# Optimization experiments

Measured on AMD Instinct MI355X. Metric: run time of the kernel, lower is better.

## Reference

```python
import jax, jax.numpy as jnp
import numpy as np

BATCH, N_IN, N_OUT, D = 32768, 256, 256, 8

def setup_inputs() -> dict:
    key = jax.random.key(0)
    k1, k2 = jax.random.split(key)
    noise_std = 1.0 / (N_IN * (D + 1))
    x = jax.random.normal(k1, (BATCH, N_IN), dtype=jnp.float32)
    c_basis = noise_std * jax.random.normal(k2, (N_OUT, N_IN, D + 1), dtype=jnp.float32)
    c_act = jnp.ones((N_OUT, N_IN), dtype=jnp.float32)
    return {"x": x, "c_basis": c_basis, "c_act": c_act}

def _cheby_basis(x, degree):
    # x: (batch, n_in) -> (batch, n_in, degree+1) Chebyshev T_k(tanh(x))
    t = jnp.tanh(x)
    polys = [jnp.ones_like(t), t]
    for _ in range(2, degree + 1):
        polys.append(2.0 * t * polys[-1] - polys[-2])
    return jnp.stack(polys[: degree + 1], axis=-1)

def reference(x, c_basis, c_act):
    batch = x.shape[0]
    n_out = c_basis.shape[0]
    degree = c_basis.shape[-1] - 1
    Ti = _cheby_basis(x, degree)                      # (batch, n_in, D+1)
    cheb = Ti.reshape(batch, -1)                      # (batch, n_in*(D+1))
    cheb_w = (c_basis * c_act[..., None]).reshape(n_out, -1)
    return jnp.matmul(cheb, cheb_w.T)                 # (batch, n_out)
```

## Files before the change

kernel.cpp:

```cpp
#include <hip/hip_runtime.h>
#include <hip/hip_bf16.h>

#define BATCH 32768
#define NIN   256
#define NOUT  256

typedef __attribute__((ext_vector_type(8))) short bf16x8;
typedef __attribute__((ext_vector_type(4))) float f32x4;
typedef __attribute__((ext_vector_type(2))) float f32x2;
typedef __attribute__((ext_vector_type(4))) unsigned int u32x4;

static __device__ __forceinline__ unsigned short bf16_rne(float f) {
  unsigned u = __float_as_uint(f);
  u += 0x7fffu + ((u >> 16) & 1u);
  return (unsigned short)(u >> 16);
}

static __device__ __forceinline__ float fast_tanh(float v) {
  float a = fabsf(v);
  float z = __expf(-2.0f * a);
  float r = (1.0f - z) * __builtin_amdgcn_rcpf(1.0f + z);
  return copysignf(r, v);
}

static __device__ __forceinline__ unsigned pack_pair(f32x2 v) {
  __hip_bfloat162 h2 = __float22bfloat162_rn(make_float2(v[0], v[1]));
  union { __hip_bfloat162 h; unsigned u; } cv;
  cv.h = h2;
  return cv.u;
}

static __device__ __forceinline__ void init_state(const f32x4 x0, const f32x4 x1,
                                                  f32x2* cur, f32x2* prev,
                                                  f32x2* t2) {
  #pragma unroll
  for (int p = 0; p < 4; ++p) {
    float va = (p < 2) ? x0[2 * p]     : x1[2 * p - 4];
    float vb = (p < 2) ? x0[2 * p + 1] : x1[2 * p - 3];
    float ta = fast_tanh(va);
    float tb = fast_tanh(vb);
    cur[p]  = (f32x2){ta, tb};
    t2[p]   = cur[p] + cur[p];
    prev[p] = (f32x2){1.0f, 1.0f};
  }
}

static __device__ __forceinline__ void phase_barrier() {
  __builtin_amdgcn_sched_barrier(0);
  __builtin_amdgcn_s_barrier();
  __builtin_amdgcn_sched_barrier(0);
}

__global__ void cheby_prepack(const float* __restrict__ cb,
                              const float* __restrict__ ca,
                              unsigned short* __restrict__ Bp) {
  int tid = blockIdx.x * 256 + threadIdx.x;
  int j    = tid & 7;
  int col  = (tid >> 3) & 15;
  int kg   = (tid >> 7) & 3;
  int tile = (tid >> 9) & 15;
  int ic   = (tid >> 13) & 7;
  int dm   = tid >> 16;
  int i = ic * 32 + kg * 8 + j;
  int n = tile * 16 + col;
  float w = cb[n * (NIN * 9) + i * 9 + (dm + 1)] * ca[n * NIN + i];
  Bp[tid] = bf16_rne(w);
}

__global__ void cheby_bias(const float* __restrict__ cb,
                           const float* __restrict__ ca,
                           float* __restrict__ bias) {
  int n = blockIdx.x;
  int l = threadIdx.x;
  float s = 0.0f;
  #pragma unroll
  for (int k = 0; k < 4; ++k) {
    int i = l + k * 64;
    s += cb[n * (NIN * 9) + i * 9] * ca[n * NIN + i];
  }
  #pragma unroll
  for (int off = 32; off; off >>= 1) s += __shfl_down(s, off);
  if (l == 0) bias[n] = s;
}

__global__ __launch_bounds__(512, 2)
void cheby_mfma(const float* __restrict__ x,
                const unsigned short* __restrict__ Bp,
                const float* __restrict__ bias,
                float* __restrict__ out) {
  __shared__ unsigned short Asm[2][8][8][512];

  int tid  = threadIdx.x;
  int w    = tid >> 6;
  int lane = tid & 63;
  int row16 = lane & 15;
  int kg    = lane >> 4;

  int wr = w >> 2;
  int wc = w & 3;
  int base_row = blockIdx.x * 128;
  int tile0    = wc * 4;

  const float* xw = x + (size_t)(base_row + w * 16 + row16) * NIN + kg * 8;
  char* wbase = (char*)Asm + (w * 1024 + lane * 16);
  const char* abase   = (const char*)Asm + lane * 16;
  const char* bp_lane = (const char*)Bp + kg * 256 + row16 * 16;

  f32x4 acc[4][4];
  #pragma unroll
  for (int a = 0; a < 4; ++a)
    #pragma unroll
    for (int b = 0; b < 4; ++b) acc[a][b] = (f32x4)0.0f;

  f32x4 xa = *(const f32x4*)xw;
  f32x4 xb = *(const f32x4*)(xw + 4);
  {
    f32x2 c0[4], p0[4], t0[4];
    init_state(xa, xb, c0, p0, t0);
    #pragma unroll
    for (int d = 1; d <= 8; ++d) {
      u32x4 pk;
      #pragma unroll
      for (int q = 0; q < 4; ++q) pk[q] = pack_pair(c0[q]);
      *(u32x4*)(wbase + (d - 1) * 8192) = pk;
      if (d < 8) {
        #pragma unroll
        for (int q = 0; q < 4; ++q) {
          f32x2 nx = __builtin_elementwise_fma(t0[q], c0[q], -p0[q]);
          p0[q] = c0[q];
          c0[q] = nx;
        }
      }
    }
  }
  xa = *(const f32x4*)(xw + 32);
  xb = *(const f32x4*)(xw + 36);
  f32x2 cur[4], prev[4], t2[4];
  init_state(xa, xb, cur, prev, t2);

  bf16x8 af[2][4], bfr[2][4];
  {
    const char* bp0 = bp_lane + (size_t)tile0 * 1024;
    #pragma unroll
    for (int nt = 0; nt < 4; ++nt)
      bfr[0][nt] = *(const bf16x8*)(bp0 + nt * 1024);
  }
  __builtin_amdgcn_sched_barrier(0);
  asm volatile("s_waitcnt lgkmcnt(0)" ::: "memory");
  __builtin_amdgcn_s_barrier();
  __builtin_amdgcn_sched_barrier(0);
  #pragma unroll
  for (int mt = 0; mt < 4; ++mt)
    af[0][mt] = *(const bf16x8*)(abase + (wr * 4 + mt) * 1024);

  for (int ic = 0; ic < 7; ++ic) {
    const char* ai   = abase + (ic & 1) * 65536 + (wr * 4) * 1024;
    const char* ain  = abase + ((ic + 1) & 1) * 65536 + (wr * 4) * 1024;
    char*       wp   = wbase + ((ic + 1) & 1) * 65536;
    const char* bpi  = bp_lane + (size_t)(ic * 16 + tile0) * 1024;
    const char* bpin = bp_lane + (size_t)((ic + 1) * 16 + tile0) * 1024;

    #pragma unroll
    for (int p = 0; p < 8; ++p) {
      if (p < 7) {
        #pragma unroll
        for (int mt = 0; mt < 4; ++mt)
          af[(p + 1) & 1][mt] =
              *(const bf16x8*)(ai + (p + 1) * 8192 + mt * 1024);
      } else {
        #pragma unroll
        for (int mt = 0; mt < 4; ++mt)
          af[0][mt] = *(const bf16x8*)(ain + mt * 1024);
      }
      if (p < 7) {
        #pragma unroll
        for (int nt = 0; nt < 4; ++nt)
          bfr[(p + 1) & 1][nt] =
              *(const bf16x8*)(bpi + (size_t)(p + 1) * 131072 + nt * 1024);
      } else {
        #pragma unroll
        for (int nt = 0; nt < 4; ++nt)
          bfr[0][nt] = *(const bf16x8*)(bpin + nt * 1024);
      }
      {
        u32x4 pk;
        #pragma unroll
        for (int q = 0; q < 4; ++q) pk[q] = pack_pair(cur[q]);
        *(u32x4*)(wp + p * 8192) = pk;
        if (p < 7) {
          #pragma unroll
          for (int q = 0; q < 4; ++q) {
            f32x2 nx = __builtin_elementwise_fma(t2[q], cur[q], -prev[q]);
            prev[q] = cur[q];
            cur[q]  = nx;
          }
        }
      }
      if (p == 3 && ic <= 5) {
        xa = *(const f32x4*)(xw + (ic + 2) * 32);
        xb = *(const f32x4*)(xw + (ic + 2) * 32 + 4);
      }
      if (p == 7 && ic <= 5)
        init_state(xa, xb, cur, prev, t2);

      phase_barrier();

      __builtin_amdgcn_s_setprio(1);
      #pragma unroll
      for (int mt = 0; mt < 4; ++mt)
        #pragma unroll
        for (int nt = 0; nt < 4; ++nt)
          acc[mt][nt] = __builtin_amdgcn_mfma_f32_16x16x32_bf16(
              af[p & 1][mt], bfr[p & 1][nt], acc[mt][nt], 0, 0, 0);
      __builtin_amdgcn_s_setprio(0);
    }
  }

  {
    const char* ai  = abase + 65536 + (wr * 4) * 1024;
    const char* bpi = bp_lane + (size_t)(7 * 16 + tile0) * 1024;
    #pragma unroll
    for (int p = 0; p < 8; ++p) {
      if (p < 7) {
        #pragma unroll
        for (int mt = 0; mt < 4; ++mt)
          af[(p + 1) & 1][mt] =
              *(const bf16x8*)(ai + (p + 1) * 8192 + mt * 1024);
        #pragma unroll
        for (int nt = 0; nt < 4; ++nt)
          bfr[(p + 1) & 1][nt] =
              *(const bf16x8*)(bpi + (size_t)(p + 1) * 131072 + nt * 1024);
      }
      __builtin_amdgcn_s_setprio(1);
      #pragma unroll
      for (int mt = 0; mt < 4; ++mt)
        #pragma unroll
        for (int nt = 0; nt < 4; ++nt)
          acc[mt][nt] = __builtin_amdgcn_mfma_f32_16x16x32_bf16(
              af[p & 1][mt], bfr[p & 1][nt], acc[mt][nt], 0, 0, 0);
      __builtin_amdgcn_s_setprio(0);
    }
  }

  #pragma unroll
  for (int nt = 0; nt < 4; ++nt) {
    int c = (tile0 + nt) * 16 + row16;
    float bv = bias[c];
    #pragma unroll
    for (int mt = 0; mt < 4; ++mt) {
      int r0 = base_row + wr * 64 + mt * 16 + kg * 4;
      #pragma unroll
      for (int q = 0; q < 4; ++q)
        out[(size_t)(r0 + q) * NOUT + c] = acc[mt][nt][q] + bv;
    }
  }
}

extern "C" void kernel_launch(void* const* d_in, const int* in_sizes, int n_in,
                              void* d_out, int out_size, void* d_ws, size_t ws_size,
                              hipStream_t stream) {
  const float* x  = (const float*)d_in[0];
  const float* cb = (const float*)d_in[1];
  const float* ca = (const float*)d_in[2];
  float* out = (float*)d_out;

  unsigned short* Bp = (unsigned short*)d_ws;
  float* bias = (float*)((char*)d_ws + 8 * NIN * NOUT * 2);

  cheby_prepack<<<(8 * NIN * NOUT) / 256, 256, 0, stream>>>(cb, ca, Bp);
  cheby_bias<<<NOUT, 64, 0, stream>>>(cb, ca, bias);
  cheby_mfma<<<256, 512, 0, stream>>>(x, Bp, bias, out);
}
```

Measured before the change: 47.75 us.

## Process two Chebyshev degrees per barrier phase, halving block barriers

The main loop now handles two degrees per phase (4 phases instead of 8 per input chunk), so each barrier is followed by 32 MFMAs instead of 16. Global B fragments are prefetched two degrees ahead in a double buffer. The A fragments are no longer software-pipelined one phase ahead: they are loaded at the start of each phase and waited on with lgkmcnt(0) right after the barrier. This cuts barrier count and increases MFMA work per sync, at the cost of more registers (B buffer doubles) and exposed LDS read latency before the MFMAs.

Result: slower. 49.43 us (+3.5%).

```diff
diff --git a/kernel.cpp b/kernel.cpp
--- a/kernel.cpp
+++ b/kernel.cpp
@@ -43,12 +43,6 @@
     t2[p]   = cur[p] + cur[p];
     prev[p] = (f32x2){1.0f, 1.0f};
   }
-}
-
-static __device__ __forceinline__ void phase_barrier() {
-  __builtin_amdgcn_sched_barrier(0);
-  __builtin_amdgcn_s_barrier();
-  __builtin_amdgcn_sched_barrier(0);
 }
 
 __global__ void cheby_prepack(const float* __restrict__ cb,
@@ -138,56 +132,59 @@
   f32x2 cur[4], prev[4], t2[4];
   init_state(xa, xb, cur, prev, t2);
 
-  bf16x8 af[2][4], bfr[2][4];
+  bf16x8 bfr[2][2][4];
   {
     const char* bp0 = bp_lane + (size_t)tile0 * 1024;
     #pragma unroll
-    for (int nt = 0; nt < 4; ++nt)
-      bfr[0][nt] = *(const bf16x8*)(bp0 + nt * 1024);
+    for (int dd = 0; dd < 2; ++dd)
+      #pragma unroll
+      for (int nt = 0; nt < 4; ++nt)
+        bfr[0][dd][nt] =
+            *(const bf16x8*)(bp0 + (size_t)dd * 131072 + nt * 1024);
   }
   __builtin_amdgcn_sched_barrier(0);
   asm volatile("s_waitcnt lgkmcnt(0)" ::: "memory");
   __builtin_amdgcn_s_barrier();
   __builtin_amdgcn_sched_barrier(0);
-  #pragma unroll
-  for (int mt = 0; mt < 4; ++mt)
-    af[0][mt] = *(const bf16x8*)(abase + (wr * 4 + mt) * 1024);
 
   for (int ic = 0; ic < 7; ++ic) {
     const char* ai   = abase + (ic & 1) * 65536 + (wr * 4) * 1024;
-    const char* ain  = abase + ((ic + 1) & 1) * 65536 + (wr * 4) * 1024;
     char*       wp   = wbase + ((ic + 1) & 1) * 65536;
     const char* bpi  = bp_lane + (size_t)(ic * 16 + tile0) * 1024;
     const char* bpin = bp_lane + (size_t)((ic + 1) * 16 + tile0) * 1024;
 
     #pragma unroll
-    for (int p = 0; p < 8; ++p) {
-      if (p < 7) {
-        #pragma unroll
-        for (int mt = 0; mt < 4; ++mt)
-          af[(p + 1) & 1][mt] =
-              *(const bf16x8*)(ai + (p + 1) * 8192 + mt * 1024);
+    for (int ph = 0; ph < 4; ++ph) {
+      const int d0 = ph * 2;
+      bf16x8 af[2][4];
+      #pragma unroll
+      for (int dd = 0; dd < 2; ++dd)
+        #pragma unroll
+        for (int mt = 0; mt < 4; ++mt)
+          af[dd][mt] =
+              *(const bf16x8*)(ai + (d0 + dd) * 8192 + mt * 1024);
+      if (ph < 3) {
+        #pragma unroll
+        for (int dd = 0; dd < 2; ++dd)
+          #pragma unroll
+          for (int nt = 0; nt < 4; ++nt)
+            bfr[(ph + 1) & 1][dd][nt] = *(const bf16x8*)(
+                bpi + (size_t)(d0 + 2 + dd) * 131072 + nt * 1024);
       } else {
         #pragma unroll
-        for (int mt = 0; mt < 4; ++mt)
-          af[0][mt] = *(const bf16x8*)(ain + mt * 1024);
-      }
-      if (p < 7) {
-        #pragma unroll
-        for (int nt = 0; nt < 4; ++nt)
-          bfr[(p + 1) & 1][nt] =
-              *(const bf16x8*)(bpi + (size_t)(p + 1) * 131072 + nt * 1024);
-      } else {
-        #pragma unroll
-        for (int nt = 0; nt < 4; ++nt)
-          bfr[0][nt] = *(const bf16x8*)(bpin + nt * 1024);
-      }
-      {
+        for (int dd = 0; dd < 2; ++dd)
+          #pragma unroll
+          for (int nt = 0; nt < 4; ++nt)
+            bfr[0][dd][nt] = *(const bf16x8*)(
+                bpin + (size_t)dd * 131072 + nt * 1024);
+      }
+      #pragma unroll
+      for (int s = 0; s < 2; ++s) {
         u32x4 pk;
         #pragma unroll
         for (int q = 0; q < 4; ++q) pk[q] = pack_pair(cur[q]);
-        *(u32x4*)(wp + p * 8192) = pk;
-        if (p < 7) {
+        *(u32x4*)(wp + (d0 + s) * 8192) = pk;
+        if (d0 + s < 7) {
           #pragma unroll
           for (int q = 0; q < 4; ++q) {
             f32x2 nx = __builtin_elementwise_fma(t2[q], cur[q], -prev[q]);
@@ -196,22 +193,27 @@
           }
         }
       }
-      if (p == 3 && ic <= 5) {
+      if (ph == 1 && ic <= 5) {
         xa = *(const f32x4*)(xw + (ic + 2) * 32);
         xb = *(const f32x4*)(xw + (ic + 2) * 32 + 4);
       }
-      if (p == 7 && ic <= 5)
+      if (ph == 3 && ic <= 5)
         init_state(xa, xb, cur, prev, t2);
 
-      phase_barrier();
+      __builtin_amdgcn_sched_barrier(0);
+      __builtin_amdgcn_s_barrier();
+      asm volatile("s_waitcnt lgkmcnt(0)" ::: "memory");
+      __builtin_amdgcn_sched_barrier(0);
 
       __builtin_amdgcn_s_setprio(1);
       #pragma unroll
-      for (int mt = 0; mt < 4; ++mt)
-        #pragma unroll
-        for (int nt = 0; nt < 4; ++nt)
-          acc[mt][nt] = __builtin_amdgcn_mfma_f32_16x16x32_bf16(
-              af[p & 1][mt], bfr[p & 1][nt], acc[mt][nt], 0, 0, 0);
+      for (int dd = 0; dd < 2; ++dd)
+        #pragma unroll
+        for (int mt = 0; mt < 4; ++mt)
+          #pragma unroll
+          for (int nt = 0; nt < 4; ++nt)
+            acc[mt][nt] = __builtin_amdgcn_mfma_f32_16x16x32_bf16(
+                af[dd][mt], bfr[ph & 1][dd][nt], acc[mt][nt], 0, 0, 0);
       __builtin_amdgcn_s_setprio(0);
     }
   }
@@ -220,24 +222,32 @@
     const char* ai  = abase + 65536 + (wr * 4) * 1024;
     const char* bpi = bp_lane + (size_t)(7 * 16 + tile0) * 1024;
     #pragma unroll
-    for (int p = 0; p < 8; ++p) {
-      if (p < 7) {
-        #pragma unroll
-        for (int mt = 0; mt < 4; ++mt)
-          af[(p + 1) & 1][mt] =
-              *(const bf16x8*)(ai + (p + 1) * 8192 + mt * 1024);
-        #pragma unroll
-        for (int nt = 0; nt < 4; ++nt)
-          bfr[(p + 1) & 1][nt] =
-              *(const bf16x8*)(bpi + (size_t)(p + 1) * 131072 + nt * 1024);
+    for (int ph = 0; ph < 4; ++ph) {
+      const int d0 = ph * 2;
+      bf16x8 af[2][4];
+      #pragma unroll
+      for (int dd = 0; dd < 2; ++dd)
+        #pragma unroll
+        for (int mt = 0; mt < 4; ++mt)
+          af[dd][mt] =
+              *(const bf16x8*)(ai + (d0 + dd) * 8192 + mt * 1024);
+      if (ph < 3) {
+        #pragma unroll
+        for (int dd = 0; dd < 2; ++dd)
+          #pragma unroll
+          for (int nt = 0; nt < 4; ++nt)
+            bfr[(ph + 1) & 1][dd][nt] = *(const bf16x8*)(
+                bpi + (size_t)(d0 + 2 + dd) * 131072 + nt * 1024);
       }
       __builtin_amdgcn_s_setprio(1);
       #pragma unroll
-      for (int mt = 0; mt < 4; ++mt)
-        #pragma unroll
-        for (int nt = 0; nt < 4; ++nt)
-          acc[mt][nt] = __builtin_amdgcn_mfma_f32_16x16x32_bf16(
-              af[p & 1][mt], bfr[p & 1][nt], acc[mt][nt], 0, 0, 0);
+      for (int dd = 0; dd < 2; ++dd)
+        #pragma unroll
+        for (int mt = 0; mt < 4; ++mt)
+          #pragma unroll
+          for (int nt = 0; nt < 4; ++nt)
+            acc[mt][nt] = __builtin_amdgcn_mfma_f32_16x16x32_bf16(
+                af[dd][mt], bfr[ph & 1][dd][nt], acc[mt][nt], 0, 0, 0);
       __builtin_amdgcn_s_setprio(0);
     }
   }
```

## Switch MFMA tiles from 16x16x32 to 32x32x16 with matching A/B layouts

Applied to the files above, without the earlier changes.

Replaces the 4x4 grid of 16x16x32 bf16 MFMAs per wave with a 2x2 grid of 32x32x16 MFMAs over two K chunks. The prepacked weight layout, the LDS A-tile layout and the epilogue row mapping change to match the 32-row fragment shape. The larger instruction is meant to issue fewer MFMAs per phase and give each fragment load more reuse. In exchange it adds new index math and a different accumulator register layout.

New measurement: 51.37 us. 1.08x slower.

```diff
diff --git a/kernel.cpp b/kernel.cpp
--- a/kernel.cpp
+++ b/kernel.cpp
@@ -5,10 +5,11 @@
 #define NIN   256
 #define NOUT  256
 
-typedef __attribute__((ext_vector_type(8))) short bf16x8;
-typedef __attribute__((ext_vector_type(4))) float f32x4;
-typedef __attribute__((ext_vector_type(2))) float f32x2;
-typedef __attribute__((ext_vector_type(4))) unsigned int u32x4;
+typedef __attribute__((ext_vector_type(8)))  short bf16x8;
+typedef __attribute__((ext_vector_type(4)))  float f32x4;
+typedef __attribute__((ext_vector_type(16))) float f32x16;
+typedef __attribute__((ext_vector_type(2)))  float f32x2;
+typedef __attribute__((ext_vector_type(4)))  unsigned int u32x4;
 
 static __device__ __forceinline__ unsigned short bf16_rne(float f) {
   unsigned u = __float_as_uint(f);
@@ -55,14 +56,16 @@
                               const float* __restrict__ ca,
                               unsigned short* __restrict__ Bp) {
   int tid = blockIdx.x * 256 + threadIdx.x;
-  int j    = tid & 7;
-  int col  = (tid >> 3) & 15;
-  int kg   = (tid >> 7) & 3;
-  int tile = (tid >> 9) & 15;
-  int ic   = (tid >> 13) & 7;
-  int dm   = tid >> 16;
-  int i = ic * 32 + kg * 8 + j;
-  int n = tile * 16 + col;
+  int j      = tid & 7;
+  int fl     = (tid >> 3) & 63;
+  int chunk  = (tid >> 9) & 1;
+  int tile32 = (tid >> 10) & 7;
+  int ic     = (tid >> 13) & 7;
+  int dm     = (tid >> 16) & 7;
+  int col = fl & 31;
+  int kh  = fl >> 5;
+  int n = tile32 * 32 + col;
+  int i = ic * 32 + chunk * 16 + kh * 8 + j;
   float w = cb[n * (NIN * 9) + i * 9 + (dm + 1)] * ca[n * NIN + i];
   Bp[tid] = bf16_rne(w);
 }
@@ -88,29 +91,27 @@
                 const unsigned short* __restrict__ Bp,
                 const float* __restrict__ bias,
                 float* __restrict__ out) {
-  __shared__ unsigned short Asm[2][8][8][512];
+  __shared__ unsigned short Asm_[2][8][4][2][512];
 
   int tid  = threadIdx.x;
   int w    = tid >> 6;
   int lane = tid & 63;
-  int row16 = lane & 15;
-  int kg    = lane >> 4;
 
   int wr = w >> 2;
   int wc = w & 3;
   int base_row = blockIdx.x * 128;
-  int tile0    = wc * 4;
-
-  const float* xw = x + (size_t)(base_row + w * 16 + row16) * NIN + kg * 8;
-  char* wbase = (char*)Asm + (w * 1024 + lane * 16);
-  const char* abase   = (const char*)Asm + lane * 16;
-  const char* bp_lane = (const char*)Bp + kg * 256 + row16 * 16;
-
-  f32x4 acc[4][4];
-  #pragma unroll
-  for (int a = 0; a < 4; ++a)
-    #pragma unroll
-    for (int b = 0; b < 4; ++b) acc[a][b] = (f32x4)0.0f;
+
+  const float* xw = x + (size_t)(base_row + ((tid >> 7) << 5) + (tid & 31)) * NIN
+                      + ((tid >> 5) & 3) * 8;
+  char* wbase = (char*)Asm_ + tid * 16;
+  const char* abase   = (const char*)Asm_ + lane * 16;
+  const char* bp_lane = (const char*)Bp + lane * 16;
+
+  f32x16 acc[2][2];
+  #pragma unroll
+  for (int a = 0; a < 2; ++a)
+    #pragma unroll
+    for (int b = 0; b < 2; ++b) acc[a][b] = (f32x16)0.0f;
 
   f32x4 xa = *(const f32x4*)xw;
   f32x4 xb = *(const f32x4*)(xw + 4);
@@ -118,12 +119,12 @@
     f32x2 c0[4], p0[4], t0[4];
     init_state(xa, xb, c0, p0, t0);
     #pragma unroll
-    for (int d = 1; d <= 8; ++d) {
+    for (int d = 0; d < 8; ++d) {
       u32x4 pk;
       #pragma unroll
       for (int q = 0; q < 4; ++q) pk[q] = pack_pair(c0[q]);
-      *(u32x4*)(wbase + (d - 1) * 8192) = pk;
-      if (d < 8) {
+      *(u32x4*)(wbase + d * 8192) = pk;
+      if (d < 7) {
         #pragma unroll
         for (int q = 0; q < 4; ++q) {
           f32x2 nx = __builtin_elementwise_fma(t0[q], c0[q], -p0[q]);
@@ -138,49 +139,64 @@
   f32x2 cur[4], prev[4], t2[4];
   init_state(xa, xb, cur, prev, t2);
 
-  bf16x8 af[2][4], bfr[2][4];
+  bf16x8 af[2][2][2], bfr[2][2][2];
   {
-    const char* bp0 = bp_lane + (size_t)tile0 * 1024;
-    #pragma unroll
-    for (int nt = 0; nt < 4; ++nt)
-      bfr[0][nt] = *(const bf16x8*)(bp0 + nt * 1024);
+    const char* bp0 = bp_lane + (size_t)(wc * 4) * 1024;
+    #pragma unroll
+    for (int ch = 0; ch < 2; ++ch)
+      #pragma unroll
+      for (int nt = 0; nt < 2; ++nt)
+        bfr[0][ch][nt] = *(const bf16x8*)(bp0 + (nt * 2 + ch) * 1024);
   }
   __builtin_amdgcn_sched_barrier(0);
   asm volatile("s_waitcnt lgkmcnt(0)" ::: "memory");
   __builtin_amdgcn_s_barrier();
   __builtin_amdgcn_sched_barrier(0);
   #pragma unroll
-  for (int mt = 0; mt < 4; ++mt)
-    af[0][mt] = *(const bf16x8*)(abase + (wr * 4 + mt) * 1024);
+  for (int mt = 0; mt < 2; ++mt)
+    #pragma unroll
+    for (int ch = 0; ch < 2; ++ch)
+      af[0][mt][ch] =
+          *(const bf16x8*)(abase + (wr * 2 + mt) * 2048 + ch * 1024);
 
   for (int ic = 0; ic < 7; ++ic) {
-    const char* ai   = abase + (ic & 1) * 65536 + (wr * 4) * 1024;
-    const char* ain  = abase + ((ic + 1) & 1) * 65536 + (wr * 4) * 1024;
+    const char* ai   = abase + (ic & 1) * 65536;
+    const char* ain  = abase + ((ic + 1) & 1) * 65536;
     char*       wp   = wbase + ((ic + 1) & 1) * 65536;
-    const char* bpi  = bp_lane + (size_t)(ic * 16 + tile0) * 1024;
-    const char* bpin = bp_lane + (size_t)((ic + 1) * 16 + tile0) * 1024;
+    const char* bpi  = bp_lane + (size_t)(ic * 16 + wc * 4) * 1024;
+    const char* bpin = bp_lane + (size_t)((ic + 1) * 16 + wc * 4) * 1024;
 
     #pragma unroll
     for (int p = 0; p < 8; ++p) {
       if (p < 7) {
         #pragma unroll
-        for (int mt = 0; mt < 4; ++mt)
-          af[(p + 1) & 1][mt] =
-              *(const bf16x8*)(ai + (p + 1) * 8192 + mt * 1024);
+        for (int mt = 0; mt < 2; ++mt)
+          #pragma unroll
+          for (int ch = 0; ch < 2; ++ch)
+            af[(p + 1) & 1][mt][ch] = *(const bf16x8*)(
+                ai + (p + 1) * 8192 + (wr * 2 + mt) * 2048 + ch * 1024);
       } else {
         #pragma unroll
-        for (int mt = 0; mt < 4; ++mt)
-          af[0][mt] = *(const bf16x8*)(ain + mt * 1024);
+        for (int mt = 0; mt < 2; ++mt)
+          #pragma unroll
+          for (int ch = 0; ch < 2; ++ch)
+            af[0][mt][ch] = *(const bf16x8*)(
+                ain + (wr * 2 + mt) * 2048 + ch * 1024);
       }
       if (p < 7) {
         #pragma unroll
-        for (int nt = 0; nt < 4; ++nt)
-          bfr[(p + 1) & 1][nt] =
-              *(const bf16x8*)(bpi + (size_t)(p + 1) * 131072 + nt * 1024);
+        for (int ch = 0; ch < 2; ++ch)
+          #pragma unroll
+          for (int nt = 0; nt < 2; ++nt)
+            bfr[(p + 1) & 1][ch][nt] = *(const bf16x8*)(
+                bpi + (size_t)(p + 1) * 131072 + (nt * 2 + ch) * 1024);
       } else {
         #pragma unroll
-        for (int nt = 0; nt < 4; ++nt)
-          bfr[0][nt] = *(const bf16x8*)(bpin + nt * 1024);
+        for (int ch = 0; ch < 2; ++ch)
+          #pragma unroll
+          for (int nt = 0; nt < 2; ++nt)
+            bfr[0][ch][nt] =
+                *(const bf16x8*)(bpin + (nt * 2 + ch) * 1024);
       }
       {
         u32x4 pk;
@@ -207,51 +223,61 @@
 
       __builtin_amdgcn_s_setprio(1);
       #pragma unroll
-      for (int mt = 0; mt < 4; ++mt)
-        #pragma unroll
-        for (int nt = 0; nt < 4; ++nt)
-          acc[mt][nt] = __builtin_amdgcn_mfma_f32_16x16x32_bf16(
-              af[p & 1][mt], bfr[p & 1][nt], acc[mt][nt], 0, 0, 0);
+      for (int ch = 0; ch < 2; ++ch)
+        #pragma unroll
+        for (int mt = 0; mt < 2; ++mt)
+          #pragma unroll
+          for (int nt = 0; nt < 2; ++nt)
+            acc[mt][nt] = __builtin_amdgcn_mfma_f32_32x32x16_bf16(
+                af[p & 1][mt][ch], bfr[p & 1][ch][nt], acc[mt][nt], 0, 0, 0);
       __builtin_amdgcn_s_setprio(0);
     }
   }
 
   {
-    const char* ai  = abase + 65536 + (wr * 4) * 1024;
-    const char* bpi = bp_lane + (size_t)(7 * 16 + tile0) * 1024;
+    const char* ai  = abase + 65536;
+    const char* bpi = bp_lane + (size_t)(7 * 16 + wc * 4) * 1024;
     #pragma unroll
     for (int p = 0; p < 8; ++p) {
       if (p < 7) {
         #pragma unroll
-        for (int mt = 0; mt < 4; ++mt)
-          af[(p + 1) & 1][mt] =
-              *(const bf16x8*)(ai + (p + 1) * 8192 + mt * 1024);
-        #pragma unroll
-        for (int nt = 0; nt < 4; ++nt)
-          bfr[(p + 1) & 1][nt] =
-              *(const bf16x8*)(bpi + (size_t)(p + 1) * 131072 + nt * 1024);
+        for (int mt = 0; mt < 2; ++mt)
+          #pragma unroll
+          for (int ch = 0; ch < 2; ++ch)
+            af[(p + 1) & 1][mt][ch] = *(const bf16x8*)(
+                ai + (p + 1) * 8192 + (wr * 2 + mt) * 2048 + ch * 1024);
+        #pragma unroll
+        for (int ch = 0; ch < 2; ++ch)
+          #pragma unroll
+          for (int nt = 0; nt < 2; ++nt)
+            bfr[(p + 1) & 1][ch][nt] = *(const bf16x8*)(
+                bpi + (size_t)(p + 1) * 131072 + (nt * 2 + ch) * 1024);
       }
       __builtin_amdgcn_s_setprio(1);
       #pragma unroll
-      for (int mt = 0; mt < 4; ++mt)
-        #pragma unroll
-        for (int nt = 0; nt < 4; ++nt)
-          acc[mt][nt] = __builtin_amdgcn_mfma_f32_16x16x32_bf16(
-              af[p & 1][mt], bfr[p & 1][nt], acc[mt][nt], 0, 0, 0);
+      for (int ch = 0; ch < 2; ++ch)
+        #pragma unroll
+        for (int mt = 0; mt < 2; ++mt)
+          #pragma unroll
+          for (int nt = 0; nt < 2; ++nt)
+            acc[mt][nt] = __builtin_amdgcn_mfma_f32_32x32x16_bf16(
+                af[p & 1][mt][ch], bfr[p & 1][ch][nt], acc[mt][nt], 0, 0, 0);
       __builtin_amdgcn_s_setprio(0);
     }
   }
 
   #pragma unroll
-  for (int nt = 0; nt < 4; ++nt) {
-    int c = (tile0 + nt) * 16 + row16;
+  for (int nt = 0; nt < 2; ++nt) {
+    int c = wc * 64 + nt * 32 + (lane & 31);
     float bv = bias[c];
     #pragma unroll
-    for (int mt = 0; mt < 4; ++mt) {
-      int r0 = base_row + wr * 64 + mt * 16 + kg * 4;
-      #pragma unroll
-      for (int q = 0; q < 4; ++q)
-        out[(size_t)(r0 + q) * NOUT + c] = acc[mt][nt][q] + bv;
+    for (int mt = 0; mt < 2; ++mt) {
+      int rbase = base_row + wr * 64 + mt * 32 + 4 * (lane >> 5);
+      #pragma unroll
+      for (int r = 0; r < 16; ++r) {
+        int row = rbase + (r & 3) + 8 * (r >> 2);
+        out[(size_t)row * NOUT + c] = acc[mt][nt][r] + bv;
+      }
     }
   }
 }
```
